# Optimization experiments

Hardware: AMD Instinct MI355X
Metric: run time of the kernel (lower is better)

Reference implementation:

```python
import jax, jax.numpy as jnp
import numpy as np

N_NODES = 50000
N_EDGES = 800000
IN_DIM = 128
OUT_DIM = 64


def setup_inputs() -> dict:
    key = jax.random.key(0)
    k1, k2, k3, k4 = jax.random.split(key, 4)
    x = jax.random.normal(k1, (N_NODES, IN_DIM), dtype=jnp.float32)
    edge_index = jax.random.randint(k2, (2, N_EDGES), 0, N_NODES, dtype=jnp.int64)
    # learned params: W: Linear(in_dim, out_dim, bias=False); att: Linear(2*out_dim, 1, bias=False)
    W = jax.random.normal(k3, (IN_DIM, OUT_DIM), dtype=jnp.float32) * 0.05
    att = jax.random.normal(k4, (2 * OUT_DIM, 1), dtype=jnp.float32) * 0.05
    return {"x": x, "edge_index": edge_index, "W": W, "att": att}


def reference(x, edge_index, W, att):
    n = x.shape[0]
    h = x @ W  # [N, D]
    src, dst = edge_index[0], edge_index[1]
    # per-edge attention logit: leaky_relu(att^T [h_src ; h_dst])
    e = jnp.concatenate([h[src], h[dst]], axis=-1) @ att  # [E, 1]
    e = jax.nn.leaky_relu(e[:, 0], negative_slope=0.2)  # [E]
    # segment softmax over edges grouped by destination node
    m = jax.ops.segment_max(e, dst, num_segments=n)  # [N]
    ex = jnp.exp(e - m[dst])  # [E]
    denom = jax.ops.segment_sum(ex, dst, num_segments=n)  # [N]
    alpha = ex / denom[dst]  # [E]
    # weighted scatter-add aggregation
    agg = jax.ops.segment_sum(alpha[:, None] * h[src], dst, num_segments=n)  # [N, D]
    return jax.nn.elu(agg)
```

## Files before the change

### kernel.cpp

```cpp
#include <hip/hip_runtime.h>
#include <hip/hip_bf16.h>
#include <hip/hip_fp16.h>
#include <math.h>

#define N_NODES 50000
#define N_EDGES 800000
#define IN_DIM 128
#define OUT_DIM 64

typedef __attribute__((ext_vector_type(8))) short bf16x8;
typedef __attribute__((ext_vector_type(4))) float f32x4;

static __device__ __forceinline__ ushort f2bf(float f) {
  uint u = __float_as_uint(f);
  uint r = (u + 0x7fffu + ((u >> 16) & 1u)) >> 16;
  return (ushort)r;
}
static __device__ __forceinline__ float bf2f(ushort h) {
  return __uint_as_float(((uint)h) << 16);
}

#define N4 (N_NODES / 4)
#define SCAN_NB ((N4 + 255) / 256)
#define GEMM_NB ((N_NODES + 63) / 64)
#define K2_T (N_EDGES / 8)
#define K4_T (N_EDGES / 8)

__global__ __launch_bounds__(256) void k0_prep(const float* __restrict__ W,
                                               int* __restrict__ deg,
                                               ushort* __restrict__ WTbf) {
  int t = blockIdx.x * 256 + threadIdx.x;
  if (t < N4) ((int4*)deg)[t] = make_int4(0, 0, 0, 0);
  if (t < IN_DIM * OUT_DIM) {
    int k = t >> 6, c = t & 63;
    WTbf[c * IN_DIM + k] = f2bf(W[t]);
  }
}

__global__ __launch_bounds__(256) void k1_mfma(
    const float* __restrict__ x, const ushort* __restrict__ WTbf,
    const float* __restrict__ att,
    __half* __restrict__ h, float* __restrict__ a1, float* __restrict__ a2) {
  int tid = threadIdx.x;
  int w = tid >> 6, l = tid & 63;
  int ml = l & 15, kg = l >> 4;
  int row0 = blockIdx.x * 64;

  int arow = row0 + w * 16 + ml;
  if (arow > N_NODES - 1) arow = N_NODES - 1;
  const float* __restrict__ xr = x + (size_t)arow * IN_DIM + kg * 8;

  bf16x8 b[4][4];
#pragma unroll
  for (int nt = 0; nt < 4; ++nt) {
    const ushort* wc = WTbf + (nt * 16 + ml) * IN_DIM + kg * 8;
#pragma unroll
    for (int ks = 0; ks < 4; ++ks)
      b[nt][ks] = *(const bf16x8*)(wc + ks * 32);
  }

  bf16x8 a_h[4], a_l[4];
#pragma unroll
  for (int ks = 0; ks < 4; ++ks) {
    float4 v0 = *(const float4*)(xr + ks * 32);
    float4 v1 = *(const float4*)(xr + ks * 32 + 4);
    float vv[8] = {v0.x, v0.y, v0.z, v0.w, v1.x, v1.y, v1.z, v1.w};
    ushort hh[8], ll[8];
#pragma unroll
    for (int q = 0; q < 8; ++q) {
      hh[q] = f2bf(vv[q]);
      ll[q] = f2bf(vv[q] - bf2f(hh[q]));
    }
    a_h[ks] = (bf16x8){(short)hh[0], (short)hh[1], (short)hh[2], (short)hh[3],
                       (short)hh[4], (short)hh[5], (short)hh[6], (short)hh[7]};
    a_l[ks] = (bf16x8){(short)ll[0], (short)ll[1], (short)ll[2], (short)ll[3],
                       (short)ll[4], (short)ll[5], (short)ll[6], (short)ll[7]};
  }

  f32x4 acc[4];
#pragma unroll
  for (int nt = 0; nt < 4; ++nt) acc[nt] = (f32x4){0.f, 0.f, 0.f, 0.f};

#pragma unroll
  for (int ks = 0; ks < 4; ++ks) {
#pragma unroll
    for (int nt = 0; nt < 4; ++nt) {
      acc[nt] = __builtin_amdgcn_mfma_f32_16x16x32_bf16(a_h[ks], b[nt][ks], acc[nt], 0, 0, 0);
      acc[nt] = __builtin_amdgcn_mfma_f32_16x16x32_bf16(a_l[ks], b[nt][ks], acc[nt], 0, 0, 0);
    }
  }

  float t1[4], t2[4];
#pragma unroll
  for (int nt = 0; nt < 4; ++nt) {
    t1[nt] = att[nt * 16 + ml];
    t2[nt] = att[OUT_DIM + nt * 16 + ml];
  }
#pragma unroll
  for (int r = 0; r < 4; ++r) {
    int drow = kg * 4 + r;
    int grow = row0 + w * 16 + drow;
    bool ok = grow < N_NODES;
    float p1 = 0.f, p2 = 0.f;
#pragma unroll
    for (int nt = 0; nt < 4; ++nt) {
      float d = acc[nt][r];
      if (ok) h[(size_t)grow * OUT_DIM + nt * 16 + ml] = __float2half(d);
      p1 = fmaf(d, t1[nt], p1);
      p2 = fmaf(d, t2[nt], p2);
    }
#pragma unroll
    for (int o = 1; o <= 8; o <<= 1) {
      p1 += __shfl_xor(p1, o, 64);
      p2 += __shfl_xor(p2, o, 64);
    }
    if (ml == 0 && ok) { a1[grow] = p1; a2[grow] = p2; }
  }
}

__global__ __launch_bounds__(256) void k2_rank(const int* __restrict__ dstp,
                                               int* __restrict__ deg,
                                               int* __restrict__ rank) {
  int t = blockIdx.x * 256 + threadIdx.x;
  if (t >= K2_T) return;
  int4 d0 = ((const int4*)dstp)[t * 2];
  int4 d1 = ((const int4*)dstp)[t * 2 + 1];
  int4 r0, r1;
  r0.x = atomicAdd(&deg[d0.x], 1);
  r0.y = atomicAdd(&deg[d0.y], 1);
  r0.z = atomicAdd(&deg[d0.z], 1);
  r0.w = atomicAdd(&deg[d0.w], 1);
  r1.x = atomicAdd(&deg[d1.x], 1);
  r1.y = atomicAdd(&deg[d1.y], 1);
  r1.z = atomicAdd(&deg[d1.z], 1);
  r1.w = atomicAdd(&deg[d1.w], 1);
  ((int4*)rank)[t * 2] = r0;
  ((int4*)rank)[t * 2 + 1] = r1;
}

__global__ __launch_bounds__(256) void k3a_scan(const int* __restrict__ deg,
                                                int* __restrict__ off,
                                                int* __restrict__ bsum) {
  __shared__ int sw[4];
  int tid = threadIdx.x, lane = tid & 63, wid = tid >> 6;
  int i4 = blockIdx.x * 256 + tid;
  int4 v = make_int4(0, 0, 0, 0);
  if (i4 < N4) v = ((const int4*)deg)[i4];
  int local = v.x + v.y + v.z + v.w;
  int incl = local;
#pragma unroll
  for (int o = 1; o < 64; o <<= 1) {
    int t = __shfl_up(incl, o, 64);
    if (lane >= o) incl += t;
  }
  if (lane == 63) sw[wid] = incl;
  __syncthreads();
  if (tid == 0) {
    int c = 0;
#pragma unroll
    for (int ww = 0; ww < 4; ++ww) { int t = sw[ww]; sw[ww] = c; c += t; }
    bsum[blockIdx.x] = c;
  }
  __syncthreads();
  int excl = incl - local + sw[wid];
  int4 o;
  o.x = excl; o.y = o.x + v.x; o.z = o.y + v.y; o.w = o.z + v.z;
  if (i4 < N4) ((int4*)off)[i4] = o;
}

__global__ __launch_bounds__(256) void k3c_add(int* __restrict__ off,
                                               const int* __restrict__ bsum,
                                               const float* __restrict__ a2,
                                               int2* __restrict__ oa2) {
  __shared__ int sb[64];
  int tid = threadIdx.x;
  if (tid < 64) {
    int v = (tid < SCAN_NB) ? bsum[tid] : 0;
    int incl = v;
#pragma unroll
    for (int o = 1; o < 64; o <<= 1) {
      int t = __shfl_up(incl, o, 64);
      if (tid >= o) incl += t;
    }
    sb[tid] = incl - v;
  }
  __syncthreads();
  int i4 = blockIdx.x * 256 + tid;
  if (i4 == 0) off[N_NODES] = N_EDGES;
  if (i4 >= N4) return;
  int add = sb[blockIdx.x];
  int4 v = ((const int4*)off)[i4];
  v.x += add; v.y += add; v.z += add; v.w += add;
  ((int4*)off)[i4] = v;
  float4 a = ((const float4*)a2)[i4];
  int4 p0 = make_int4(v.x, __float_as_int(a.x), v.y, __float_as_int(a.y));
  int4 p1 = make_int4(v.z, __float_as_int(a.z), v.w, __float_as_int(a.w));
  ((int4*)oa2)[i4 * 2] = p0;
  ((int4*)oa2)[i4 * 2 + 1] = p1;
}

__global__ __launch_bounds__(256) void k4_scatter(
    const int* __restrict__ src, const int* __restrict__ dstp,
    const int* __restrict__ rank,
    const float* __restrict__ a1, const int2* __restrict__ oa2,
    int2* __restrict__ sedge) {
  int t = blockIdx.x * 256 + threadIdx.x;
  if (t >= K4_T) return;
  int4 s0 = ((const int4*)src)[t * 2],  s1 = ((const int4*)src)[t * 2 + 1];
  int4 d0 = ((const int4*)dstp)[t * 2], d1 = ((const int4*)dstp)[t * 2 + 1];
  int4 r0 = ((const int4*)rank)[t * 2], r1 = ((const int4*)rank)[t * 2 + 1];
  float A[8];
  A[0] = a1[s0.x]; A[1] = a1[s0.y]; A[2] = a1[s0.z]; A[3] = a1[s0.w];
  A[4] = a1[s1.x]; A[5] = a1[s1.y]; A[6] = a1[s1.z]; A[7] = a1[s1.w];
  int2 O[8];
  O[0] = oa2[d0.x]; O[1] = oa2[d0.y]; O[2] = oa2[d0.z]; O[3] = oa2[d0.w];
  O[4] = oa2[d1.x]; O[5] = oa2[d1.y]; O[6] = oa2[d1.z]; O[7] = oa2[d1.w];
  int S[8] = {s0.x, s0.y, s0.z, s0.w, s1.x, s1.y, s1.z, s1.w};
  int R[8] = {r0.x, r0.y, r0.z, r0.w, r1.x, r1.y, r1.z, r1.w};
#pragma unroll
  for (int q = 0; q < 8; ++q) {
    float e = A[q] + __int_as_float(O[q].y);
    e = e > 0.f ? e : 0.2f * e;
    sedge[O[q].x + R[q]] = make_int2(S[q], __float_as_int(__expf(e)));
  }
}

__global__ __launch_bounds__(256) void k5_agg(
    const int* __restrict__ off, const int2* __restrict__ sedge,
    const __half* __restrict__ h, float* __restrict__ out) {
  int tid = threadIdx.x;
  int g = tid >> 3, gl = tid & 7;
  int n = blockIdx.x * 32 + g;
  if (n >= N_NODES) return;
  int b = off[n], e = off[n + 1];

  float sum = 0.f;
  float a0 = 0.f, a1_ = 0.f, a2_ = 0.f, a3 = 0.f;
  float a4 = 0.f, a5 = 0.f, a6 = 0.f, a7 = 0.f;
  const __half* __restrict__ hb = h;

#define K5_ACC(rr, ww)                                                        \
  {                                                                           \
    float2 f;                                                                 \
    f = __half22float2(__builtin_bit_cast(__half2, rr.x));                    \
    a0 = fmaf(ww, f.x, a0); a1_ = fmaf(ww, f.y, a1_);                         \
    f = __half22float2(__builtin_bit_cast(__half2, rr.y));                    \
    a2_ = fmaf(ww, f.x, a2_); a3 = fmaf(ww, f.y, a3);                         \
    f = __half22float2(__builtin_bit_cast(__half2, rr.z));                    \
    a4 = fmaf(ww, f.x, a4); a5 = fmaf(ww, f.y, a5);                           \
    f = __half22float2(__builtin_bit_cast(__half2, rr.w));                    \
    a6 = fmaf(ww, f.x, a6); a7 = fmaf(ww, f.y, a7);                           \
  }

  int j = b;
  for (; j + 7 < e; j += 8) {
    int2 s0 = sedge[j + 0], s1 = sedge[j + 1], s2 = sedge[j + 2], s3 = sedge[j + 3];
    int2 s4 = sedge[j + 4], s5 = sedge[j + 5], s6 = sedge[j + 6], s7 = sedge[j + 7];
    uint4 r0 = ((const uint4*)(hb + (size_t)s0.x * OUT_DIM))[gl];
    uint4 r1 = ((const uint4*)(hb + (size_t)s1.x * OUT_DIM))[gl];
    uint4 r2 = ((const uint4*)(hb + (size_t)s2.x * OUT_DIM))[gl];
    uint4 r3 = ((const uint4*)(hb + (size_t)s3.x * OUT_DIM))[gl];
    uint4 r4 = ((const uint4*)(hb + (size_t)s4.x * OUT_DIM))[gl];
    uint4 r5 = ((const uint4*)(hb + (size_t)s5.x * OUT_DIM))[gl];
    uint4 r6 = ((const uint4*)(hb + (size_t)s6.x * OUT_DIM))[gl];
    uint4 r7 = ((const uint4*)(hb + (size_t)s7.x * OUT_DIM))[gl];
    float w0 = __int_as_float(s0.y), w1 = __int_as_float(s1.y);
    float w2 = __int_as_float(s2.y), w3 = __int_as_float(s3.y);
    float w4 = __int_as_float(s4.y), w5 = __int_as_float(s5.y);
    float w6 = __int_as_float(s6.y), w7 = __int_as_float(s7.y);
    sum += ((w0 + w1) + (w2 + w3)) + ((w4 + w5) + (w6 + w7));
    K5_ACC(r0, w0); K5_ACC(r1, w1); K5_ACC(r2, w2); K5_ACC(r3, w3);
    K5_ACC(r4, w4); K5_ACC(r5, w5); K5_ACC(r6, w6); K5_ACC(r7, w7);
  }
  for (; j + 3 < e; j += 4) {
    int2 s0 = sedge[j + 0], s1 = sedge[j + 1], s2 = sedge[j + 2], s3 = sedge[j + 3];
    uint4 r0 = ((const uint4*)(hb + (size_t)s0.x * OUT_DIM))[gl];
    uint4 r1 = ((const uint4*)(hb + (size_t)s1.x * OUT_DIM))[gl];
    uint4 r2 = ((const uint4*)(hb + (size_t)s2.x * OUT_DIM))[gl];
    uint4 r3 = ((const uint4*)(hb + (size_t)s3.x * OUT_DIM))[gl];
    float w0 = __int_as_float(s0.y), w1 = __int_as_float(s1.y);
    float w2 = __int_as_float(s2.y), w3 = __int_as_float(s3.y);
    sum += (w0 + w1) + (w2 + w3);
    K5_ACC(r0, w0); K5_ACC(r1, w1); K5_ACC(r2, w2); K5_ACC(r3, w3);
  }
  for (; j < e; ++j) {
    int2 s0 = sedge[j];
    uint4 r0 = ((const uint4*)(hb + (size_t)s0.x * OUT_DIM))[gl];
    float w0 = __int_as_float(s0.y);
    sum += w0;
    K5_ACC(r0, w0);
  }

  float inv = (e > b) ? 1.f / sum : 0.f;
  a0 *= inv; a1_ *= inv; a2_ *= inv; a3 *= inv;
  a4 *= inv; a5 *= inv; a6 *= inv; a7 *= inv;
  float4 o0, o1;
  o0.x = a0 > 0.f ? a0 : (__expf(a0) - 1.f);
  o0.y = a1_ > 0.f ? a1_ : (__expf(a1_) - 1.f);
  o0.z = a2_ > 0.f ? a2_ : (__expf(a2_) - 1.f);
  o0.w = a3 > 0.f ? a3 : (__expf(a3) - 1.f);
  o1.x = a4 > 0.f ? a4 : (__expf(a4) - 1.f);
  o1.y = a5 > 0.f ? a5 : (__expf(a5) - 1.f);
  o1.z = a6 > 0.f ? a6 : (__expf(a6) - 1.f);
  o1.w = a7 > 0.f ? a7 : (__expf(a7) - 1.f);
  float4* ob = (float4*)(out + (size_t)n * OUT_DIM);
  ob[gl * 2] = o0;
  ob[gl * 2 + 1] = o1;
}

extern "C" void kernel_launch(void* const* d_in, const int* in_sizes, int n_in,
                              void* d_out, int out_size, void* d_ws, size_t ws_size,
                              hipStream_t stream) {
  const float* x   = (const float*)d_in[0];
  const int*   ei  = (const int*)d_in[1];
  const float* W   = (const float*)d_in[2];
  const float* att = (const float*)d_in[3];
  float* out = (float*)d_out;

  char* p = (char*)d_ws;
  __half* h  = (__half*)p;  p += (size_t)N_NODES * OUT_DIM * sizeof(__half);
  float* a1  = (float*)p;   p += (size_t)N_NODES * sizeof(float);
  float* a2  = (float*)p;   p += (size_t)N_NODES * sizeof(float);
  int*   deg = (int*)p;     p += (size_t)N_NODES * sizeof(int);
  int*   off = (int*)p;     p += (size_t)(N_NODES + 4) * sizeof(int);
  int2*  oa2 = (int2*)p;    p += (size_t)N_NODES * sizeof(int2);
  int*   rank = (int*)p;    p += (size_t)N_EDGES * sizeof(int);
  int2*  sedge = (int2*)p;  p += (size_t)N_EDGES * sizeof(int2);
  int*   bsum = (int*)p;    p += 64 * sizeof(int);
  ushort* WTbf = (ushort*)p; p += (size_t)OUT_DIM * IN_DIM * sizeof(ushort);

  const int* src  = ei;
  const int* dstp = ei + N_EDGES;

  k0_prep<<<SCAN_NB, 256, 0, stream>>>(W, deg, WTbf);
  k2_rank<<<(K2_T + 255) / 256, 256, 0, stream>>>(dstp, deg, rank);
  k1_mfma<<<GEMM_NB, 256, 0, stream>>>(x, WTbf, att, h, a1, a2);
  k3a_scan<<<SCAN_NB, 256, 0, stream>>>(deg, off, bsum);
  k3c_add<<<SCAN_NB, 256, 0, stream>>>(off, bsum, a2, oa2);
  k4_scatter<<<(K4_T + 255) / 256, 256, 0, stream>>>(src, dstp, rank, a1, oa2, sedge);
  k5_agg<<<(N_NODES + 31) / 32, 256, 0, stream>>>(off, sedge, h, out);
}
```

Measured before the change: 103.6 us.

## Stage x tile through swizzled LDS and prepack W into MFMA fragment order

The GEMM kernel now loads the x tile with fully coalesced float4 reads, splits each value into bf16 hi/lo parts and stores them in XOR-swizzled shared memory, then reads MFMA A fragments from LDS. W is pre-packed by the prep kernel directly into per-lane fragment order, so each lane's B load is one contiguous 16-byte read. This replaces strided per-lane global loads of x and W and is meant to improve memory coalescing in the GEMM stage. In exchange it adds 32 KB of LDS per block, which may limit occupancy, and a block-wide barrier.

```diff
diff --git a/kernel.cpp b/kernel.cpp
--- a/kernel.cpp
+++ b/kernel.cpp
@@ -28,65 +28,65 @@
 
 __global__ __launch_bounds__(256) void k0_prep(const float* __restrict__ W,
                                                int* __restrict__ deg,
-                                               ushort* __restrict__ WTbf) {
+                                               ushort* __restrict__ WTfrag) {
   int t = blockIdx.x * 256 + threadIdx.x;
   if (t < N4) ((int4*)deg)[t] = make_int4(0, 0, 0, 0);
   if (t < IN_DIM * OUT_DIM) {
-    int k = t >> 6, c = t & 63;
-    WTbf[c * IN_DIM + k] = f2bf(W[t]);
+    int j = t & 7, l = (t >> 3) & 63, ks = (t >> 9) & 3, nt = (t >> 11) & 3;
+    int c = nt * 16 + (l & 15);
+    int k = ks * 32 + ((l >> 4) << 3) + j;
+    WTfrag[t] = f2bf(W[(size_t)k * OUT_DIM + c]);
   }
 }
 
 __global__ __launch_bounds__(256) void k1_mfma(
-    const float* __restrict__ x, const ushort* __restrict__ WTbf,
+    const float* __restrict__ x, const ushort* __restrict__ WTfrag,
     const float* __restrict__ att,
     __half* __restrict__ h, float* __restrict__ a1, float* __restrict__ a2) {
+  __shared__ __align__(16) ushort Ah[64 * 128];
+  __shared__ __align__(16) ushort Al[64 * 128];
+
   int tid = threadIdx.x;
+  int row0 = blockIdx.x * 64;
+
+#pragma unroll
+  for (int it = 0; it < 8; ++it) {
+    int i4 = it * 256 + tid;
+    int row = i4 >> 5;
+    int kq = i4 & 31;
+    int grow = row0 + row;
+    if (grow > N_NODES - 1) grow = N_NODES - 1;
+    float4 v = ((const float4*)x)[(size_t)grow * 32 + kq];
+    ushort4 hi, lo;
+    hi.x = f2bf(v.x); lo.x = f2bf(v.x - bf2f(hi.x));
+    hi.y = f2bf(v.y); lo.y = f2bf(v.y - bf2f(hi.y));
+    hi.z = f2bf(v.z); lo.z = f2bf(v.z - bf2f(hi.z));
+    hi.w = f2bf(v.w); lo.w = f2bf(v.w - bf2f(hi.w));
+    int idx = (row * 128 + kq * 4) ^ ((row & 7) << 3);
+    *(ushort4*)&Ah[idx] = hi;
+    *(ushort4*)&Al[idx] = lo;
+  }
+  __syncthreads();
+
   int w = tid >> 6, l = tid & 63;
   int ml = l & 15, kg = l >> 4;
-  int row0 = blockIdx.x * 64;
-
-  int arow = row0 + w * 16 + ml;
-  if (arow > N_NODES - 1) arow = N_NODES - 1;
-  const float* __restrict__ xr = x + (size_t)arow * IN_DIM + kg * 8;
-
-  bf16x8 b[4][4];
-#pragma unroll
-  for (int nt = 0; nt < 4; ++nt) {
-    const ushort* wc = WTbf + (nt * 16 + ml) * IN_DIM + kg * 8;
-#pragma unroll
-    for (int ks = 0; ks < 4; ++ks)
-      b[nt][ks] = *(const bf16x8*)(wc + ks * 32);
-  }
-
-  bf16x8 a_h[4], a_l[4];
+  const bf16x8* __restrict__ Bf = (const bf16x8*)WTfrag;
+
+  f32x4 acc[4];
+#pragma unroll
+  for (int nt = 0; nt < 4; ++nt) acc[nt] = (f32x4){0.f, 0.f, 0.f, 0.f};
+
 #pragma unroll
   for (int ks = 0; ks < 4; ++ks) {
-    float4 v0 = *(const float4*)(xr + ks * 32);
-    float4 v1 = *(const float4*)(xr + ks * 32 + 4);
-    float vv[8] = {v0.x, v0.y, v0.z, v0.w, v1.x, v1.y, v1.z, v1.w};
-    ushort hh[8], ll[8];
-#pragma unroll
-    for (int q = 0; q < 8; ++q) {
-      hh[q] = f2bf(vv[q]);
-      ll[q] = f2bf(vv[q] - bf2f(hh[q]));
-    }
-    a_h[ks] = (bf16x8){(short)hh[0], (short)hh[1], (short)hh[2], (short)hh[3],
-                       (short)hh[4], (short)hh[5], (short)hh[6], (short)hh[7]};
-    a_l[ks] = (bf16x8){(short)ll[0], (short)ll[1], (short)ll[2], (short)ll[3],
-                       (short)ll[4], (short)ll[5], (short)ll[6], (short)ll[7]};
-  }
-
-  f32x4 acc[4];
-#pragma unroll
-  for (int nt = 0; nt < 4; ++nt) acc[nt] = (f32x4){0.f, 0.f, 0.f, 0.f};
-
-#pragma unroll
-  for (int ks = 0; ks < 4; ++ks) {
+    int arow = w * 16 + ml;
+    int aidx = (arow * 128 + ks * 32 + kg * 8) ^ ((arow & 7) << 3);
+    bf16x8 a_h = *(const bf16x8*)&Ah[aidx];
+    bf16x8 a_l = *(const bf16x8*)&Al[aidx];
 #pragma unroll
     for (int nt = 0; nt < 4; ++nt) {
-      acc[nt] = __builtin_amdgcn_mfma_f32_16x16x32_bf16(a_h[ks], b[nt][ks], acc[nt], 0, 0, 0);
-      acc[nt] = __builtin_amdgcn_mfma_f32_16x16x32_bf16(a_l[ks], b[nt][ks], acc[nt], 0, 0, 0);
+      bf16x8 b = Bf[(nt * 4 + ks) * 64 + l];
+      acc[nt] = __builtin_amdgcn_mfma_f32_16x16x32_bf16(a_h, b, acc[nt], 0, 0, 0);
+      acc[nt] = __builtin_amdgcn_mfma_f32_16x16x32_bf16(a_l, b, acc[nt], 0, 0, 0);
     }
   }
 
@@ -327,14 +327,14 @@
   int*   rank = (int*)p;    p += (size_t)N_EDGES * sizeof(int);
   int2*  sedge = (int2*)p;  p += (size_t)N_EDGES * sizeof(int2);
   int*   bsum = (int*)p;    p += 64 * sizeof(int);
-  ushort* WTbf = (ushort*)p; p += (size_t)OUT_DIM * IN_DIM * sizeof(ushort);
+  ushort* WTfrag = (ushort*)p; p += (size_t)OUT_DIM * IN_DIM * sizeof(ushort);
 
   const int* src  = ei;
   const int* dstp = ei + N_EDGES;
 
-  k0_prep<<<SCAN_NB, 256, 0, stream>>>(W, deg, WTbf);
+  k0_prep<<<SCAN_NB, 256, 0, stream>>>(W, deg, WTfrag);
   k2_rank<<<(K2_T + 255) / 256, 256, 0, stream>>>(dstp, deg, rank);
-  k1_mfma<<<GEMM_NB, 256, 0, stream>>>(x, WTbf, att, h, a1, a2);
+  k1_mfma<<<GEMM_NB, 256, 0, stream>>>(x, WTfrag, att, h, a1, a2);
   k3a_scan<<<SCAN_NB, 256, 0, stream>>>(deg, off, bsum);
   k3c_add<<<SCAN_NB, 256, 0, stream>>>(off, bsum, a2, oa2);
   k4_scatter<<<(K4_T + 255) / 256, 256, 0, stream>>>(src, dstp, rank, a1, oa2, sedge);
```

Result: faster. 98.39 us (-5.0%).
